# Kernel tuning notes

Hardware: AMD Instinct MI355X
Metric: run time of the kernel (lower is better)

## Reference

```python
import jax, jax.numpy as jnp
import numpy as np

B, S, D = 1, 2048, 2048      # batch, seq, hidden_dim
DF = 768                      # moe intermediate (per routed expert)
DSH = 2048                    # shared-expert intermediate
E, K = 32, 8                  # num routed experts, top_k
BLK = 128                     # fp8 block-scale size
CAP = 1024
T = B * S


def _dequant(w, s, blk=BLK):
    # w: [E, M, N] fp8 values (stored fp32), s: [E, M/blk, N/blk] block scales
    Eh, M, N = w.shape
    Mb, Nb = s.shape[1], s.shape[2]
    return (w.reshape(Eh, Mb, blk, Nb, blk) * s[:, :, None, :, None]).reshape(Eh, M, N)


def setup_inputs() -> dict:
    key = jax.random.key(0)
    ks = jax.random.split(key, 13)
    n = lambda k, shp, sc=0.02: jax.random.normal(k, shp, jnp.float32) * sc
    u = lambda k, shp: jax.random.uniform(k, shp, jnp.float32, 0.005, 0.02)
    return {
        "hidden_states": jax.random.normal(ks[0], (B, S, D), jnp.float32),
        "router_w": n(ks[1], (E, D)),
        # raw fp8-value weights (simulated as fp32 integers-in-range values) + block scale_inv
        "wg_fp8": jax.random.normal(ks[2], (E, DF, D), jnp.float32),
        "sg": u(ks[3], (E, DF // BLK, D // BLK)),
        "wu_fp8": jax.random.normal(ks[4], (E, DF, D), jnp.float32),
        "su": u(ks[5], (E, DF // BLK, D // BLK)),
        "wd_fp8": jax.random.normal(ks[6], (E, D, DF), jnp.float32),
        "sd": u(ks[7], (E, D // BLK, DF // BLK)),
        "ws_gate": n(ks[8], (DSH, D)),
        "ws_up": n(ks[9], (DSH, D)),
        "ws_down": n(ks[10], (D, DSH)),
        "w_shared_gate": n(ks[11], (1, D)),
    }


def reference(hidden_states, router_w, wg_fp8, sg, wu_fp8, su, wd_fp8, sd,
              ws_gate, ws_up, ws_down, w_shared_gate):
    x = hidden_states.reshape(-1, D)  # [T, D]

    # shared expert (SwiGLU) + its sigmoid gate
    shared = (jax.nn.silu(x @ ws_gate.T) * (x @ ws_up.T)) @ ws_down.T
    sh_gate = jax.nn.sigmoid(x @ w_shared_gate.T)  # [T, 1]

    # router: softmax -> top-k -> renormalize (Qwen MoE gate)
    probs = jax.nn.softmax(x @ router_w.T, axis=-1)          # [T, E]
    rw, sel = jax.lax.top_k(probs, K)                        # [T, K]
    rw = rw / jnp.sum(rw, axis=-1, keepdims=True)

    # capacity-based dispatch (replaces the python per-expert loop; same math)
    flat_e = sel.reshape(-1)                                 # [T*K]
    oh = jax.nn.one_hot(flat_e, E, dtype=jnp.int32)
    pos = jnp.sum(jnp.cumsum(oh, axis=0) * oh, axis=-1) - 1  # position within expert
    keep = (pos < CAP)
    pos_c = jnp.minimum(pos, CAP)                            # overflow -> scratch slot CAP
    tok = jnp.arange(T * K) // K                             # owning token of each (t,k) pair

    buf = jnp.zeros((E, CAP + 1, D), x.dtype).at[flat_e, pos_c].set(x[tok])

    # block-scale dequant (fp8*scale_inv), then per-expert SwiGLU
    Wg = _dequant(wg_fp8, sg)
    Wu = _dequant(wu_fp8, su)
    Wd = _dequant(wd_fp8, sd)
    g = jnp.einsum('ecd,efd->ecf', buf, Wg)
    up = jnp.einsum('ecd,efd->ecf', buf, Wu)
    h = jax.nn.silu(g) * up
    y = jnp.einsum('ecf,edf->ecd', h, Wd)                    # [E, CAP+1, D]

    # weighted scatter-add back to tokens (index_add_ equivalent)
    y_tok = y[flat_e, pos_c]                                 # [T*K, D]
    w_tok = rw.reshape(-1) * keep.astype(x.dtype)
    out = jax.ops.segment_sum(y_tok * w_tok[:, None], tok, num_segments=T)

    out = out + sh_gate * shared
    return out.reshape(B, S, D)
```

## Files before the change

### kernel.cpp

```cpp
#include <hip/hip_runtime.h>
#include <hip/hip_bf16.h>


#define TT   2048
#define DD   2048
#define DFF  768
#define DSH  2048
#define EE   32
#define KTOP 8
#define CAP  1024

typedef _Float16 half8  __attribute__((ext_vector_type(8)));
typedef _Float16 half4v __attribute__((ext_vector_type(4)));
typedef float    f32x4  __attribute__((ext_vector_type(4)));

__global__ __launch_bounds__(256) void k_init(int* __restrict__ cnt,
                                              int* __restrict__ slot_tok) {
  int i = blockIdx.x * 256 + threadIdx.x;
  if (i < EE * CAP) slot_tok[i] = 0;
  if (i < EE) cnt[i] = 0;
}

__global__ __launch_bounds__(256) void k_cast(const float* __restrict__ in,
                                              _Float16* __restrict__ out) {
  int i = blockIdx.x * 256 + threadIdx.x;
  float4 v = ((const float4*)in)[i];
  half4v h = { (_Float16)v.x, (_Float16)v.y, (_Float16)v.z, (_Float16)v.w };
  ((half4v*)out)[i] = h;
}

__global__ __launch_bounds__(64) void k_router(
    const float* __restrict__ x, const float* __restrict__ rw,
    const float* __restrict__ wshg,
    float* __restrict__ shg, int* __restrict__ cnt,
    int* __restrict__ slot_tok, float* __restrict__ slot_w,
    int* __restrict__ slot_pair, int* __restrict__ pair_pos) {
  int t = blockIdx.x;
  int lane = threadIdx.x;
  const float* xr = x + (size_t)t * DD;
  float xv[32];
#pragma unroll
  for (int j = 0; j < 32; ++j) xv[j] = xr[lane + j * 64];

  __shared__ float lg[EE];
  for (int e = 0; e < EE; ++e) {
    const float* we = rw + (size_t)e * DD;
    float s = 0.f;
#pragma unroll
    for (int j = 0; j < 32; ++j) s += xv[j] * we[lane + j * 64];
#pragma unroll
    for (int off = 32; off > 0; off >>= 1) s += __shfl_down(s, off);
    if (lane == 0) lg[e] = s;
  }
  {
    float s = 0.f;
#pragma unroll
    for (int j = 0; j < 32; ++j) s += xv[j] * wshg[lane + j * 64];
#pragma unroll
    for (int off = 32; off > 0; off >>= 1) s += __shfl_down(s, off);
    if (lane == 0) shg[t] = 1.f / (1.f + expf(-s));
  }
  if (lane == 0) {
    unsigned used = 0;
    int sel[KTOP];
    float val[KTOP];
    for (int k = 0; k < KTOP; ++k) {
      float bv = -1e30f; int bi = 0;
      for (int e = 0; e < EE; ++e)
        if (!((used >> e) & 1) && lg[e] > bv) { bv = lg[e]; bi = e; }
      used |= (1u << bi);
      sel[k] = bi; val[k] = bv;
    }
    float mx = val[0], sum = 0.f;
    for (int k = 0; k < KTOP; ++k) { val[k] = expf(val[k] - mx); sum += val[k]; }
    float inv = 1.f / sum;
    for (int k = 0; k < KTOP; ++k) {
      int e = sel[k];
      int pos = atomicAdd(&cnt[e], 1);
      pair_pos[t * KTOP + k] = pos;
      if (pos < CAP) {
        slot_tok[e * CAP + pos] = t;
        slot_w[e * CAP + pos] = val[k] * inv;
        slot_pair[e * CAP + pos] = t * KTOP + k;
      }
    }
  }
}

template<bool DUAL, bool GATHER, int EPI, int NPB, int MBB, int KDIM>
__global__ __launch_bounds__(256, 2) void k_gemm(
    const _Float16* __restrict__ A,
    const float* __restrict__ B0f, const float* __restrict__ B1f,
    const float* __restrict__ S0, const float* __restrict__ S1,
    int sCols, int sStrideE,
    _Float16* __restrict__ OutH,
    int ldA, int ldOut,
    long long strideAE, long long strideBE, long long strideOE,
    const int* __restrict__ cnt,
    const int* __restrict__ slot_tok, const float* __restrict__ slot_w) {
  constexpr int BK = 64;
  constexpr int KT = KDIM / BK;
  constexpr int NF = DUAL ? 2 : 4;
  constexpr int BN = DUAL ? 64 : 128;
  constexpr int BCH = DUAL ? 4 : 8;

  const int f = blockIdx.x;
  const int xcd = f & 7;
  const int t0 = f >> 3;
  const int mb = t0 % MBB;
  const int pp = t0 / MBB;
  const int p  = pp * 8 + xcd;
  const int nb = p % NPB;
  const int e  = p / NPB;

  int rows = cnt[e] > CAP ? CAP : cnt[e];
  const int rowBase = mb * 128;
  if (rowBase >= rows) return;
  const int nBase = nb * BN;

  const int tid = threadIdx.x;
  const int lane = tid & 63;
  const int wave = tid >> 6;
  const int wr = wave >> 1;
  const int wc = wave & 1;

  __shared__ __align__(16) _Float16 sA[3][8192];
  __shared__ __align__(16) _Float16 sB[2][8192];

  const _Float16* Ae = A + (GATHER ? 0 : (long long)e * strideAE);
  const float* B0e = B0f + (long long)e * strideBE;
  const float* B1e = DUAL ? (B1f + (long long)e * strideBE) : nullptr;
  const float* S0e = S0 + (long long)e * sStrideE;
  const float* S1e = DUAL ? (S1 + (long long)e * sStrideE) : nullptr;
  const int sRow = (nBase >> 7) * sCols;

  int aByte[4];
#pragma unroll
  for (int i = 0; i < 4; ++i) {
    int c = tid + i * 256;
    int row = c >> 3;
    int colB = ((c & 7) << 4) ^ ((row & 7) << 4);
    int src = GATHER ? slot_tok[e * CAP + rowBase + row] : (rowBase + row);
    aByte[i] = src * (2 * ldA) + colB;
  }
  int bOff[BCH], wByte[BCH];
#pragma unroll
  for (int i = 0; i < BCH; ++i) {
    int c = tid + i * 256;
    int rn = c >> 4;
    int c4 = (c & 15) << 2;
    bOff[i] = (nBase + rn) * KDIM + c4;
    wByte[i] = ((rn << 7) + (c4 << 1)) ^ ((rn & 7) << 4);
  }

  f32x4 accG[4][NF];
  f32x4 accU[DUAL ? 4 : 1][NF];
#pragma unroll
  for (int m = 0; m < 4; ++m)
#pragma unroll
    for (int n = 0; n < NF; ++n) {
      accG[m][n] = (f32x4){0.f, 0.f, 0.f, 0.f};
      if constexpr (DUAL) accU[m][n] = (f32x4){0.f, 0.f, 0.f, 0.f};
    }

  auto stageA = [&](int kt, int buf) {
#pragma unroll
    for (int i = 0; i < 4; ++i) {
      __builtin_amdgcn_global_load_lds(
          (const __attribute__((address_space(1))) void*)
              ((const char*)Ae + aByte[i] + kt * (BK * 2)),
          (__attribute__((address_space(3))) void*)&sA[buf][(tid + i * 256) * 8],
          16, 0, 0);
    }
  };
  auto loadB = [&](int kt, float4 (&r0)[BCH], float4 (&r1)[BCH]) {
    const int ko = kt * BK;
#pragma unroll
    for (int i = 0; i < BCH; ++i) r0[i] = *(const float4*)(B0e + bOff[i] + ko);
    if constexpr (DUAL) {
#pragma unroll
      for (int i = 0; i < BCH; ++i) r1[i] = *(const float4*)(B1e + bOff[i] + ko);
    }
  };
  auto storeB = [&](int kt, float4 (&r0)[BCH], float4 (&r1)[BCH]) {
    float s0 = S0e[sRow + (kt >> 1)];
    float s1 = DUAL ? S1e[sRow + (kt >> 1)] : 0.f;
    char* base = (char*)&sB[kt & 1][0];
#pragma unroll
    for (int i = 0; i < BCH; ++i) {
      half4v h = { (_Float16)(r0[i].x * s0), (_Float16)(r0[i].y * s0),
                   (_Float16)(r0[i].z * s0), (_Float16)(r0[i].w * s0) };
      *(half4v*)(base + wByte[i]) = h;
      if constexpr (DUAL) {
        half4v h1 = { (_Float16)(r1[i].x * s1), (_Float16)(r1[i].y * s1),
                      (_Float16)(r1[i].z * s1), (_Float16)(r1[i].w * s1) };
        *(half4v*)(base + 8192 + wByte[i]) = h1;
      }
    }
  };
  auto computeTile = [&](int ia, int ib) {
    const char* pA = (const char*)&sA[ia][0];
    const char* pB = (const char*)&sB[ib][0];
#pragma unroll
    for (int kk = 0; kk < 2; ++kk) {
      const int koff = kk * 32 + (lane >> 4) * 8;
      half8 a[4];
#pragma unroll
      for (int m = 0; m < 4; ++m) {
        int r = wr * 64 + m * 16 + (lane & 15);
        int byt = ((r << 7) + (koff << 1)) ^ ((r & 7) << 4);
        a[m] = *(const half8*)(pA + byt);
      }
      if constexpr (DUAL) {
        half8 bg[2], bu[2];
#pragma unroll
        for (int n = 0; n < 2; ++n) {
          int rn = wc * 32 + n * 16 + (lane & 15);
          int byt = ((rn << 7) + (koff << 1)) ^ ((rn & 7) << 4);
          bg[n] = *(const half8*)(pB + byt);
          bu[n] = *(const half8*)(pB + 8192 + byt);
        }
#pragma unroll
        for (int m = 0; m < 4; ++m)
#pragma unroll
          for (int n = 0; n < 2; ++n) {
            accG[m][n] = __builtin_amdgcn_mfma_f32_16x16x32_f16(a[m], bg[n], accG[m][n], 0, 0, 0);
            accU[m][n] = __builtin_amdgcn_mfma_f32_16x16x32_f16(a[m], bu[n], accU[m][n], 0, 0, 0);
          }
      } else {
        half8 b[4];
#pragma unroll
        for (int n = 0; n < 4; ++n) {
          int rn = wc * 64 + n * 16 + (lane & 15);
          int byt = ((rn << 7) + (koff << 1)) ^ ((rn & 7) << 4);
          b[n] = *(const half8*)(pB + byt);
        }
#pragma unroll
        for (int m = 0; m < 4; ++m)
#pragma unroll
          for (int n = 0; n < 4; ++n)
            accG[m][n] = __builtin_amdgcn_mfma_f32_16x16x32_f16(a[m], b[n], accG[m][n], 0, 0, 0);
      }
    }
  };

  float4 rbE0[BCH], rbE1[BCH], rbO0[BCH], rbO1[BCH];

  loadB(0, rbE0, rbE1);
  loadB(1, rbO0, rbO1);
  stageA(0, 0);
  stageA(1, 1);
  __builtin_amdgcn_sched_barrier(0);
  storeB(0, rbE0, rbE1);
  asm volatile("s_waitcnt lgkmcnt(0)" ::: "memory");
  asm volatile("s_waitcnt vmcnt(4)" ::: "memory");
  __builtin_amdgcn_s_barrier();
  __builtin_amdgcn_sched_barrier(0);

  int bufC = 0, bufW = 2;
  for (int kt = 0; kt < KT; ++kt) {
    if (kt + 2 < KT) {
      stageA(kt + 2, bufW);
      if (kt & 1) loadB(kt + 2, rbO0, rbO1);
      else        loadB(kt + 2, rbE0, rbE1);
      __builtin_amdgcn_sched_barrier(0);
    }
    computeTile(bufC, kt & 1);
    if (kt + 1 < KT) {
      if (kt & 1) storeB(kt + 1, rbE0, rbE1);
      else        storeB(kt + 1, rbO0, rbO1);
    }
    asm volatile("s_waitcnt lgkmcnt(0)" ::: "memory");
    if (kt + 2 < KT) { asm volatile("s_waitcnt vmcnt(12)" ::: "memory"); }
    else             { asm volatile("s_waitcnt vmcnt(0)"  ::: "memory"); }
    __builtin_amdgcn_s_barrier();
    __builtin_amdgcn_sched_barrier(0);
    bufC = (bufC == 2) ? 0 : bufC + 1;
    bufW = (bufW == 2) ? 0 : bufW + 1;
  }

#pragma unroll
  for (int m = 0; m < 4; ++m) {
#pragma unroll
    for (int i = 0; i < 4; ++i) {
      int row = rowBase + wr * 64 + m * 16 + (lane >> 4) * 4 + i;
      if (row < rows) {
        if constexpr (EPI == 1) {
          int pair = slot_tok[e * CAP + row];
          float w = slot_w[e * CAP + row];
#pragma unroll
          for (int n = 0; n < NF; ++n) {
            int col = nBase + wc * 64 + n * 16 + (lane & 15);
            OutH[(long long)pair * DD + col] = (_Float16)(w * accG[m][n][i]);
          }
        } else {
          long long outBase = (long long)e * strideOE;
#pragma unroll
          for (int n = 0; n < NF; ++n) {
            int col = nBase + (DUAL ? wc * 32 : wc * 64) + n * 16 + (lane & 15);
            long long o = outBase + (long long)row * ldOut + col;
            if constexpr (DUAL) {
              float gv = accG[m][n][i];
              float uv = accU[m][n][i];
              OutH[o] = (_Float16)((gv / (1.f + __expf(-gv))) * uv);
            } else {
              OutH[o] = (_Float16)accG[m][n][i];
            }
          }
        }
      }
    }
  }
}

template<bool DUAL, int EPI, int NPB, int MBB, int KDIM>
__global__ __launch_bounds__(256, 2) void k_gemm16(
    const _Float16* __restrict__ A,
    const _Float16* __restrict__ B0h, const _Float16* __restrict__ B1h,
    _Float16* __restrict__ OutH, float* __restrict__ OutF,
    const float* __restrict__ shg,
    int ldA, int ldOut, int rowsConst) {
  constexpr int BK = 64;
  constexpr int KT = KDIM / BK;
  constexpr int NF = DUAL ? 2 : 4;
  constexpr int BN = DUAL ? 64 : 128;

  const int f = blockIdx.x;
  const int xcd = f & 7;
  const int t0 = f >> 3;
  const int mb = t0 % MBB;
  const int pp = t0 / MBB;
  const int p  = pp * 8 + xcd;
  const int nb = p % NPB;

  int rows = rowsConst;
  const int rowBase = mb * 128;
  if (rowBase >= rows) return;
  const int nBase = nb * BN;

  const int tid = threadIdx.x;
  const int lane = tid & 63;
  const int wave = tid >> 6;
  const int wr = wave >> 1;
  const int wc = wave & 1;

  __shared__ __align__(16) _Float16 sA[3][8192];
  __shared__ __align__(16) _Float16 sB[2][8192];

  int aByte[4];
#pragma unroll
  for (int i = 0; i < 4; ++i) {
    int c = tid + i * 256;
    int row = c >> 3;
    int colB = ((c & 7) << 4) ^ ((row & 7) << 4);
    aByte[i] = (rowBase + row) * (2 * ldA) + colB;
  }
  int bByte[4];
#pragma unroll
  for (int i = 0; i < 4; ++i) {
    int c = tid + i * 256;
    int rn = DUAL ? ((c & 511) >> 3) : (c >> 3);
    int colB = ((c & 7) << 4) ^ ((rn & 7) << 4);
    bByte[i] = (nBase + rn) * (2 * KDIM) + colB;
  }

  f32x4 accG[4][NF];
  f32x4 accU[DUAL ? 4 : 1][NF];
#pragma unroll
  for (int m = 0; m < 4; ++m)
#pragma unroll
    for (int n = 0; n < NF; ++n) {
      accG[m][n] = (f32x4){0.f, 0.f, 0.f, 0.f};
      if constexpr (DUAL) accU[m][n] = (f32x4){0.f, 0.f, 0.f, 0.f};
    }

  auto stageA = [&](int kt, int buf) {
#pragma unroll
    for (int i = 0; i < 4; ++i) {
      __builtin_amdgcn_global_load_lds(
          (const __attribute__((address_space(1))) void*)
              ((const char*)A + aByte[i] + kt * 128),
          (__attribute__((address_space(3))) void*)&sA[buf][(tid + i * 256) * 8],
          16, 0, 0);
    }
  };
  auto stageB = [&](int kt, int buf) {
#pragma unroll
    for (int i = 0; i < 4; ++i) {
      const _Float16* src = (DUAL && i >= 2) ? B1h : B0h;
      __builtin_amdgcn_global_load_lds(
          (const __attribute__((address_space(1))) void*)
              ((const char*)src + bByte[i] + kt * 128),
          (__attribute__((address_space(3))) void*)&sB[buf][(tid + i * 256) * 8],
          16, 0, 0);
    }
  };
  auto computeTile = [&](int ia, int ib) {
    const char* pA = (const char*)&sA[ia][0];
    const char* pB = (const char*)&sB[ib][0];
#pragma unroll
    for (int kk = 0; kk < 2; ++kk) {
      const int koff = kk * 32 + (lane >> 4) * 8;
      half8 a[4];
#pragma unroll
      for (int m = 0; m < 4; ++m) {
        int r = wr * 64 + m * 16 + (lane & 15);
        int byt = ((r << 7) + (koff << 1)) ^ ((r & 7) << 4);
        a[m] = *(const half8*)(pA + byt);
      }
      if constexpr (DUAL) {
        half8 bg[2], bu[2];
#pragma unroll
        for (int n = 0; n < 2; ++n) {
          int rn = wc * 32 + n * 16 + (lane & 15);
          int byt = ((rn << 7) + (koff << 1)) ^ ((rn & 7) << 4);
          bg[n] = *(const half8*)(pB + byt);
          bu[n] = *(const half8*)(pB + 8192 + byt);
        }
#pragma unroll
        for (int m = 0; m < 4; ++m)
#pragma unroll
          for (int n = 0; n < 2; ++n) {
            accG[m][n] = __builtin_amdgcn_mfma_f32_16x16x32_f16(a[m], bg[n], accG[m][n], 0, 0, 0);
            accU[m][n] = __builtin_amdgcn_mfma_f32_16x16x32_f16(a[m], bu[n], accU[m][n], 0, 0, 0);
          }
      } else {
        half8 b[4];
#pragma unroll
        for (int n = 0; n < 4; ++n) {
          int rn = wc * 64 + n * 16 + (lane & 15);
          int byt = ((rn << 7) + (koff << 1)) ^ ((rn & 7) << 4);
          b[n] = *(const half8*)(pB + byt);
        }
#pragma unroll
        for (int m = 0; m < 4; ++m)
#pragma unroll
          for (int n = 0; n < 4; ++n)
            accG[m][n] = __builtin_amdgcn_mfma_f32_16x16x32_f16(a[m], b[n], accG[m][n], 0, 0, 0);
      }
    }
  };

  stageB(0, 0);
  __builtin_amdgcn_sched_barrier(0);
  stageA(0, 0);
  __builtin_amdgcn_sched_barrier(0);
  stageA(1, 1);
  __builtin_amdgcn_sched_barrier(0);

  int bufC = 0, bufW = 2;
  for (int kt = 0; kt < KT; ++kt) {
    asm volatile("s_waitcnt lgkmcnt(0)" ::: "memory");
    if (kt + 1 < KT) { asm volatile("s_waitcnt vmcnt(4)" ::: "memory"); }
    else             { asm volatile("s_waitcnt vmcnt(0)" ::: "memory"); }
    __builtin_amdgcn_sched_barrier(0);
    __builtin_amdgcn_s_barrier();
    __builtin_amdgcn_sched_barrier(0);
    if (kt + 1 < KT) stageB(kt + 1, (kt + 1) & 1);
    if (kt + 2 < KT) stageA(kt + 2, bufW);
    __builtin_amdgcn_sched_barrier(0);
    computeTile(bufC, kt & 1);
    bufC = (bufC == 2) ? 0 : bufC + 1;
    bufW = (bufW == 2) ? 0 : bufW + 1;
  }

#pragma unroll
  for (int m = 0; m < 4; ++m) {
#pragma unroll
    for (int i = 0; i < 4; ++i) {
      int row = rowBase + wr * 64 + m * 16 + (lane >> 4) * 4 + i;
      if (row < rows) {
        if constexpr (EPI == 2) {
          float g = shg[row];
#pragma unroll
          for (int n = 0; n < NF; ++n) {
            int col = nBase + wc * 64 + n * 16 + (lane & 15);
            OutF[(long long)row * DD + col] += g * accG[m][n][i];
          }
        } else {
#pragma unroll
          for (int n = 0; n < NF; ++n) {
            int col = nBase + (DUAL ? wc * 32 : wc * 64) + n * 16 + (lane & 15);
            long long o = (long long)row * ldOut + col;
            if constexpr (DUAL) {
              float gv = accG[m][n][i];
              float uv = accU[m][n][i];
              OutH[o] = (_Float16)((gv / (1.f + __expf(-gv))) * uv);
            } else {
              OutH[o] = (_Float16)accG[m][n][i];
            }
          }
        }
      }
    }
  }
}

__global__ __launch_bounds__(256) void k_combine(
    const _Float16* __restrict__ Yp, const int* __restrict__ pair_pos,
    float* __restrict__ out) {
  int t = blockIdx.x;
  int col = threadIdx.x * 8;
  float acc[8] = {0.f, 0.f, 0.f, 0.f, 0.f, 0.f, 0.f, 0.f};
#pragma unroll
  for (int k = 0; k < KTOP; ++k) {
    if (pair_pos[t * KTOP + k] < CAP) {
      half8 y = *(const half8*)&Yp[((size_t)t * KTOP + k) * DD + col];
#pragma unroll
      for (int j = 0; j < 8; ++j) acc[j] += (float)y[j];
    }
  }
  float4 o0 = {acc[0], acc[1], acc[2], acc[3]};
  float4 o1 = {acc[4], acc[5], acc[6], acc[7]};
  *(float4*)&out[(size_t)t * DD + col] = o0;
  *(float4*)&out[(size_t)t * DD + col + 4] = o1;
}

extern "C" void kernel_launch(void* const* d_in, const int* in_sizes, int n_in,
                              void* d_out, int out_size, void* d_ws, size_t ws_size,
                              hipStream_t stream) {
  (void)in_sizes; (void)n_in; (void)out_size; (void)ws_size;
  const float* x    = (const float*)d_in[0];
  const float* rw   = (const float*)d_in[1];
  const float* wg   = (const float*)d_in[2];
  const float* sg   = (const float*)d_in[3];
  const float* wu   = (const float*)d_in[4];
  const float* su   = (const float*)d_in[5];
  const float* wd   = (const float*)d_in[6];
  const float* sd   = (const float*)d_in[7];
  const float* wsg  = (const float*)d_in[8];
  const float* wsu  = (const float*)d_in[9];
  const float* wsd  = (const float*)d_in[10];
  const float* wshg = (const float*)d_in[11];
  float* out = (float*)d_out;

  char* p = (char*)d_ws;
  auto alloc = [&](size_t bytes) {
    char* r = p;
    p += (bytes + 255) & ~(size_t)255;
    return r;
  };
  _Float16* x_h   = (_Float16*)alloc((size_t)TT * DD * 2);
  _Float16* H     = (_Float16*)alloc((size_t)EE * CAP * DFF * 2);
  _Float16* Hsh   = (_Float16*)alloc((size_t)TT * DSH * 2);
  _Float16* Yp    = (_Float16*)alloc((size_t)TT * KTOP * DD * 2);
  _Float16* wsg_h = (_Float16*)alloc((size_t)DSH * DD * 2);
  _Float16* wsu_h = (_Float16*)alloc((size_t)DSH * DD * 2);
  _Float16* wsd_h = (_Float16*)alloc((size_t)DD * DSH * 2);
  float* shg      = (float*)alloc((size_t)TT * 4);
  int* cnt        = (int*)alloc((size_t)EE * 4);
  int* slot_tok   = (int*)alloc((size_t)EE * CAP * 4);
  float* slot_w   = (float*)alloc((size_t)EE * CAP * 4);
  int* slot_pair  = (int*)alloc((size_t)EE * CAP * 4);
  int* pair_pos   = (int*)alloc((size_t)TT * KTOP * 4);

  k_init<<<(EE * CAP + 255) / 256, 256, 0, stream>>>(cnt, slot_tok);
  k_cast<<<(TT * DD / 4) / 256, 256, 0, stream>>>(x, x_h);
  k_cast<<<(DSH * DD / 4) / 256, 256, 0, stream>>>(wsg, wsg_h);
  k_cast<<<(DSH * DD / 4) / 256, 256, 0, stream>>>(wsu, wsu_h);
  k_cast<<<(DD * DSH / 4) / 256, 256, 0, stream>>>(wsd, wsd_h);
  k_router<<<TT, 64, 0, stream>>>(x, rw, wshg, shg, cnt, slot_tok, slot_w,
                                  slot_pair, pair_pos);

  k_gemm<true, true, 0, 12, 8, DD><<<3072, 256, 0, stream>>>(
      x_h, wg, wu, sg, su, DD / 128, (DFF / 128) * (DD / 128),
      H, DD, DFF,
      0LL, (long long)DFF * DD, (long long)CAP * DFF,
      cnt, slot_tok, nullptr);

  k_gemm<false, false, 1, 16, 8, DFF><<<4096, 256, 0, stream>>>(
      H, wd, wd, sd, sd, DFF / 128, (DD / 128) * (DFF / 128),
      Yp, DFF, DD,
      (long long)CAP * DFF, (long long)DD * DFF, 0LL,
      cnt, slot_pair, slot_w);

  k_combine<<<TT, 256, 0, stream>>>(Yp, pair_pos, out);

  k_gemm16<true, 0, 32, 16, DD><<<512, 256, 0, stream>>>(
      x_h, wsg_h, wsu_h, Hsh, nullptr, nullptr,
      DD, DSH, TT);

  k_gemm16<false, 2, 16, 16, DSH><<<256, 256, 0, stream>>>(
      Hsh, wsd_h, wsd_h, nullptr, out, shg,
      DSH, DD, TT);
}
```

Measured before the change: 762.2 us.

## Fold weight dequant/cast into idle gate-up GEMM blocks via work pool

Early-exit and finished blocks of the gate/up expert GEMM now pull chunks from an atomic work counter and use them to dequantize the down-projection weights and cast the shared-expert weights to fp16. This lets the separate cast kernels go away. The down-projection GEMM then runs on the pre-dequantized fp16 weights through the generic fp16 GEMM path, which was extended to handle per-expert strides and gather. The gate/up pipeline is also restructured into a two-step unrolled loop with different wait and barrier placement. The cost is a larger fp16 workspace, extra writes of the dequantized weights, and added work at the tail of the GEMM kernel.

```diff
diff --git a/kernel.cpp b/kernel.cpp
--- a/kernel.cpp
+++ b/kernel.cpp
@@ -14,11 +14,18 @@
 typedef _Float16 half4v __attribute__((ext_vector_type(4)));
 typedef float    f32x4  __attribute__((ext_vector_type(4)));
 
+#define N4_WD  12582912LL
+#define N4_SH  1048576LL
+#define PCHUNK 8192
+#define NCHUNK 1920
+
 __global__ __launch_bounds__(256) void k_init(int* __restrict__ cnt,
-                                              int* __restrict__ slot_tok) {
+                                              int* __restrict__ slot_tok,
+                                              int* __restrict__ ctr) {
   int i = blockIdx.x * 256 + threadIdx.x;
   if (i < EE * CAP) slot_tok[i] = 0;
   if (i < EE) cnt[i] = 0;
+  if (i == 0) *ctr = 0;
 }
 
 __global__ __launch_bounds__(256) void k_cast(const float* __restrict__ in,
@@ -87,22 +94,69 @@
   }
 }
 
-template<bool DUAL, bool GATHER, int EPI, int NPB, int MBB, int KDIM>
-__global__ __launch_bounds__(256, 2) void k_gemm(
+__device__ __forceinline__ void pool_fn(
+    int tid, int* lds_c, int* ctr,
+    const float* __restrict__ wd, const float* __restrict__ sd,
+    _Float16* __restrict__ wd_h,
+    const float* __restrict__ wsg, const float* __restrict__ wsu,
+    const float* __restrict__ wsd,
+    _Float16* __restrict__ wsg_h, _Float16* __restrict__ wsu_h,
+    _Float16* __restrict__ wsd_h) {
+  __syncthreads();
+  for (;;) {
+    if (tid == 0) *lds_c = atomicAdd(ctr, 1);
+    __syncthreads();
+    int c = *lds_c;
+    __syncthreads();
+    if (c >= NCHUNK) return;
+    long long base = (long long)c * PCHUNK;
+    for (int j = 0; j < PCHUNK / 256; ++j) {
+      long long idx = base + tid + j * 256;
+      if (idx < N4_WD) {
+        long long b = idx * 4;
+        int e = (int)(b / ((long long)DD * DFF));
+        int rem = (int)(b - (long long)e * DD * DFF);
+        int r = rem / DFF;
+        int col = rem - r * DFF;
+        float sc = sd[e * ((DD / 128) * (DFF / 128)) +
+                      (r >> 7) * (DFF / 128) + (col >> 7)];
+        float4 v = ((const float4*)wd)[idx];
+        half4v h = { (_Float16)(v.x * sc), (_Float16)(v.y * sc),
+                     (_Float16)(v.z * sc), (_Float16)(v.w * sc) };
+        ((half4v*)wd_h)[idx] = h;
+      } else {
+        long long i2 = idx - N4_WD;
+        const float* src; _Float16* dst;
+        if (i2 < N4_SH)            { src = wsg; dst = wsg_h; }
+        else if (i2 < 2 * N4_SH)   { src = wsu; dst = wsu_h; i2 -= N4_SH; }
+        else                       { src = wsd; dst = wsd_h; i2 -= 2 * N4_SH; }
+        float4 v = ((const float4*)src)[i2];
+        half4v h = { (_Float16)v.x, (_Float16)v.y, (_Float16)v.z, (_Float16)v.w };
+        ((half4v*)dst)[i2] = h;
+      }
+    }
+  }
+}
+
+template<int NPB, int MBB, int KDIM>
+__global__ __launch_bounds__(256, 2) void k_gemm_gu(
     const _Float16* __restrict__ A,
     const float* __restrict__ B0f, const float* __restrict__ B1f,
     const float* __restrict__ S0, const float* __restrict__ S1,
     int sCols, int sStrideE,
     _Float16* __restrict__ OutH,
-    int ldA, int ldOut,
-    long long strideAE, long long strideBE, long long strideOE,
-    const int* __restrict__ cnt,
-    const int* __restrict__ slot_tok, const float* __restrict__ slot_w) {
+    int ldA, int ldOut, long long strideBE, long long strideOE,
+    const int* __restrict__ cnt, const int* __restrict__ slot_tok,
+    int* __restrict__ ctr,
+    const float* __restrict__ pwd, const float* __restrict__ psd,
+    _Float16* __restrict__ pwd_h,
+    const float* __restrict__ pwsg, const float* __restrict__ pwsu,
+    const float* __restrict__ pwsd,
+    _Float16* __restrict__ pwsg_h, _Float16* __restrict__ pwsu_h,
+    _Float16* __restrict__ pwsd_h) {
   constexpr int BK = 64;
   constexpr int KT = KDIM / BK;
-  constexpr int NF = DUAL ? 2 : 4;
-  constexpr int BN = DUAL ? 64 : 128;
-  constexpr int BCH = DUAL ? 4 : 8;
+  constexpr int BCH = 4;
 
   const int f = blockIdx.x;
   const int xcd = f & 7;
@@ -113,25 +167,30 @@
   const int nb = p % NPB;
   const int e  = p / NPB;
 
+  const int tid = threadIdx.x;
+
+  __shared__ __align__(16) _Float16 sA[3][8192];
+  __shared__ __align__(16) _Float16 sB[2][8192];
+  int* lds_c = (int*)&sA[0][0];
+
   int rows = cnt[e] > CAP ? CAP : cnt[e];
   const int rowBase = mb * 128;
-  if (rowBase >= rows) return;
-  const int nBase = nb * BN;
-
-  const int tid = threadIdx.x;
+  if (rowBase >= rows) {
+    pool_fn(tid, lds_c, ctr, pwd, psd, pwd_h, pwsg, pwsu, pwsd,
+            pwsg_h, pwsu_h, pwsd_h);
+    return;
+  }
+  const int nBase = nb * 64;
+
   const int lane = tid & 63;
   const int wave = tid >> 6;
   const int wr = wave >> 1;
   const int wc = wave & 1;
 
-  __shared__ __align__(16) _Float16 sA[3][8192];
-  __shared__ __align__(16) _Float16 sB[2][8192];
-
-  const _Float16* Ae = A + (GATHER ? 0 : (long long)e * strideAE);
   const float* B0e = B0f + (long long)e * strideBE;
-  const float* B1e = DUAL ? (B1f + (long long)e * strideBE) : nullptr;
+  const float* B1e = B1f + (long long)e * strideBE;
   const float* S0e = S0 + (long long)e * sStrideE;
-  const float* S1e = DUAL ? (S1 + (long long)e * sStrideE) : nullptr;
+  const float* S1e = S1 + (long long)e * sStrideE;
   const int sRow = (nBase >> 7) * sCols;
 
   int aByte[4];
@@ -140,7 +199,7 @@
     int c = tid + i * 256;
     int row = c >> 3;
     int colB = ((c & 7) << 4) ^ ((row & 7) << 4);
-    int src = GATHER ? slot_tok[e * CAP + rowBase + row] : (rowBase + row);
+    int src = slot_tok[e * CAP + rowBase + row];
     aByte[i] = src * (2 * ldA) + colB;
   }
   int bOff[BCH], wByte[BCH];
@@ -153,14 +212,13 @@
     wByte[i] = ((rn << 7) + (c4 << 1)) ^ ((rn & 7) << 4);
   }
 
-  f32x4 accG[4][NF];
-  f32x4 accU[DUAL ? 4 : 1][NF];
+  f32x4 accG[4][2], accU[4][2];
 #pragma unroll
   for (int m = 0; m < 4; ++m)
 #pragma unroll
-    for (int n = 0; n < NF; ++n) {
+    for (int n = 0; n < 2; ++n) {
       accG[m][n] = (f32x4){0.f, 0.f, 0.f, 0.f};
-      if constexpr (DUAL) accU[m][n] = (f32x4){0.f, 0.f, 0.f, 0.f};
+      accU[m][n] = (f32x4){0.f, 0.f, 0.f, 0.f};
     }
 
   auto stageA = [&](int kt, int buf) {
@@ -168,7 +226,7 @@
     for (int i = 0; i < 4; ++i) {
       __builtin_amdgcn_global_load_lds(
           (const __attribute__((address_space(1))) void*)
-              ((const char*)Ae + aByte[i] + kt * (BK * 2)),
+              ((const char*)A + aByte[i] + kt * (BK * 2)),
           (__attribute__((address_space(3))) void*)&sA[buf][(tid + i * 256) * 8],
           16, 0, 0);
     }
@@ -177,25 +235,21 @@
     const int ko = kt * BK;
 #pragma unroll
     for (int i = 0; i < BCH; ++i) r0[i] = *(const float4*)(B0e + bOff[i] + ko);
-    if constexpr (DUAL) {
-#pragma unroll
-      for (int i = 0; i < BCH; ++i) r1[i] = *(const float4*)(B1e + bOff[i] + ko);
-    }
+#pragma unroll
+    for (int i = 0; i < BCH; ++i) r1[i] = *(const float4*)(B1e + bOff[i] + ko);
   };
   auto storeB = [&](int kt, float4 (&r0)[BCH], float4 (&r1)[BCH]) {
     float s0 = S0e[sRow + (kt >> 1)];
-    float s1 = DUAL ? S1e[sRow + (kt >> 1)] : 0.f;
+    float s1 = S1e[sRow + (kt >> 1)];
     char* base = (char*)&sB[kt & 1][0];
 #pragma unroll
     for (int i = 0; i < BCH; ++i) {
       half4v h = { (_Float16)(r0[i].x * s0), (_Float16)(r0[i].y * s0),
                    (_Float16)(r0[i].z * s0), (_Float16)(r0[i].w * s0) };
       *(half4v*)(base + wByte[i]) = h;
-      if constexpr (DUAL) {
-        half4v h1 = { (_Float16)(r1[i].x * s1), (_Float16)(r1[i].y * s1),
-                      (_Float16)(r1[i].z * s1), (_Float16)(r1[i].w * s1) };
-        *(half4v*)(base + 8192 + wByte[i]) = h1;
-      }
+      half4v h1 = { (_Float16)(r1[i].x * s1), (_Float16)(r1[i].y * s1),
+                    (_Float16)(r1[i].z * s1), (_Float16)(r1[i].w * s1) };
+      *(half4v*)(base + 8192 + wByte[i]) = h1;
     }
   };
   auto computeTile = [&](int ia, int ib) {
@@ -211,70 +265,58 @@
         int byt = ((r << 7) + (koff << 1)) ^ ((r & 7) << 4);
         a[m] = *(const half8*)(pA + byt);
       }
-      if constexpr (DUAL) {
-        half8 bg[2], bu[2];
+      half8 bg[2], bu[2];
+#pragma unroll
+      for (int n = 0; n < 2; ++n) {
+        int rn = wc * 32 + n * 16 + (lane & 15);
+        int byt = ((rn << 7) + (koff << 1)) ^ ((rn & 7) << 4);
+        bg[n] = *(const half8*)(pB + byt);
+        bu[n] = *(const half8*)(pB + 8192 + byt);
+      }
+#pragma unroll
+      for (int m = 0; m < 4; ++m)
 #pragma unroll
         for (int n = 0; n < 2; ++n) {
-          int rn = wc * 32 + n * 16 + (lane & 15);
-          int byt = ((rn << 7) + (koff << 1)) ^ ((rn & 7) << 4);
-          bg[n] = *(const half8*)(pB + byt);
-          bu[n] = *(const half8*)(pB + 8192 + byt);
+          accG[m][n] = __builtin_amdgcn_mfma_f32_16x16x32_f16(a[m], bg[n], accG[m][n], 0, 0, 0);
+          accU[m][n] = __builtin_amdgcn_mfma_f32_16x16x32_f16(a[m], bu[n], accU[m][n], 0, 0, 0);
         }
-#pragma unroll
-        for (int m = 0; m < 4; ++m)
-#pragma unroll
-          for (int n = 0; n < 2; ++n) {
-            accG[m][n] = __builtin_amdgcn_mfma_f32_16x16x32_f16(a[m], bg[n], accG[m][n], 0, 0, 0);
-            accU[m][n] = __builtin_amdgcn_mfma_f32_16x16x32_f16(a[m], bu[n], accU[m][n], 0, 0, 0);
-          }
-      } else {
-        half8 b[4];
-#pragma unroll
-        for (int n = 0; n < 4; ++n) {
-          int rn = wc * 64 + n * 16 + (lane & 15);
-          int byt = ((rn << 7) + (koff << 1)) ^ ((rn & 7) << 4);
-          b[n] = *(const half8*)(pB + byt);
-        }
-#pragma unroll
-        for (int m = 0; m < 4; ++m)
-#pragma unroll
-          for (int n = 0; n < 4; ++n)
-            accG[m][n] = __builtin_amdgcn_mfma_f32_16x16x32_f16(a[m], b[n], accG[m][n], 0, 0, 0);
-      }
     }
   };
 
   float4 rbE0[BCH], rbE1[BCH], rbO0[BCH], rbO1[BCH];
 
-  loadB(0, rbE0, rbE1);
-  loadB(1, rbO0, rbO1);
-  stageA(0, 0);
-  stageA(1, 1);
+  stageA(0, 0); loadB(0, rbE0, rbE1);
   __builtin_amdgcn_sched_barrier(0);
-  storeB(0, rbE0, rbE1);
-  asm volatile("s_waitcnt lgkmcnt(0)" ::: "memory");
-  asm volatile("s_waitcnt vmcnt(4)" ::: "memory");
-  __builtin_amdgcn_s_barrier();
+  stageA(1, 1); loadB(1, rbO0, rbO1);
   __builtin_amdgcn_sched_barrier(0);
 
   int bufC = 0, bufW = 2;
-  for (int kt = 0; kt < KT; ++kt) {
-    if (kt + 2 < KT) {
-      stageA(kt + 2, bufW);
-      if (kt & 1) loadB(kt + 2, rbO0, rbO1);
-      else        loadB(kt + 2, rbE0, rbE1);
-      __builtin_amdgcn_sched_barrier(0);
-    }
-    computeTile(bufC, kt & 1);
-    if (kt + 1 < KT) {
-      if (kt & 1) storeB(kt + 1, rbE0, rbE1);
-      else        storeB(kt + 1, rbO0, rbO1);
-    }
+  for (int kt = 0; kt < KT; kt += 2) {
+    if (kt + 1 < KT) { asm volatile("s_waitcnt vmcnt(12)" ::: "memory"); }
+    else             { asm volatile("s_waitcnt vmcnt(0)"  ::: "memory"); }
+    __builtin_amdgcn_sched_barrier(0);
+    storeB(kt, rbE0, rbE1);
     asm volatile("s_waitcnt lgkmcnt(0)" ::: "memory");
+    __builtin_amdgcn_sched_barrier(0);
+    __builtin_amdgcn_s_barrier();
+    __builtin_amdgcn_sched_barrier(0);
+    if (kt + 2 < KT) { stageA(kt + 2, bufW); loadB(kt + 2, rbE0, rbE1); }
+    __builtin_amdgcn_sched_barrier(0);
+    computeTile(bufC, 0);
+    bufC = (bufC == 2) ? 0 : bufC + 1;
+    bufW = (bufW == 2) ? 0 : bufW + 1;
+
     if (kt + 2 < KT) { asm volatile("s_waitcnt vmcnt(12)" ::: "memory"); }
     else             { asm volatile("s_waitcnt vmcnt(0)"  ::: "memory"); }
+    __builtin_amdgcn_sched_barrier(0);
+    storeB(kt + 1, rbO0, rbO1);
+    asm volatile("s_waitcnt lgkmcnt(0)" ::: "memory");
+    __builtin_amdgcn_sched_barrier(0);
     __builtin_amdgcn_s_barrier();
     __builtin_amdgcn_sched_barrier(0);
+    if (kt + 3 < KT) { stageA(kt + 3, bufW); loadB(kt + 3, rbO0, rbO1); }
+    __builtin_amdgcn_sched_barrier(0);
+    computeTile(bufC, 1);
     bufC = (bufC == 2) ? 0 : bufC + 1;
     bufW = (bufW == 2) ? 0 : bufW + 1;
   }
@@ -285,43 +327,33 @@
     for (int i = 0; i < 4; ++i) {
       int row = rowBase + wr * 64 + m * 16 + (lane >> 4) * 4 + i;
       if (row < rows) {
-        if constexpr (EPI == 1) {
-          int pair = slot_tok[e * CAP + row];
-          float w = slot_w[e * CAP + row];
-#pragma unroll
-          for (int n = 0; n < NF; ++n) {
-            int col = nBase + wc * 64 + n * 16 + (lane & 15);
-            OutH[(long long)pair * DD + col] = (_Float16)(w * accG[m][n][i]);
-          }
-        } else {
-          long long outBase = (long long)e * strideOE;
-#pragma unroll
-          for (int n = 0; n < NF; ++n) {
-            int col = nBase + (DUAL ? wc * 32 : wc * 64) + n * 16 + (lane & 15);
-            long long o = outBase + (long long)row * ldOut + col;
-            if constexpr (DUAL) {
-              float gv = accG[m][n][i];
-              float uv = accU[m][n][i];
-              OutH[o] = (_Float16)((gv / (1.f + __expf(-gv))) * uv);
-            } else {
-              OutH[o] = (_Float16)accG[m][n][i];
-            }
-          }
+#pragma unroll
+        for (int n = 0; n < 2; ++n) {
+          int col = nBase + wc * 32 + n * 16 + (lane & 15);
+          float gv = accG[m][n][i];
+          float uv = accU[m][n][i];
+          OutH[(long long)e * strideOE + (long long)row * ldOut + col] =
+              (_Float16)((gv / (1.f + __expf(-gv))) * uv);
         }
       }
     }
   }
-}
-
-template<bool DUAL, int EPI, int NPB, int MBB, int KDIM>
+
+  pool_fn(tid, lds_c, ctr, pwd, psd, pwd_h, pwsg, pwsu, pwsd,
+          pwsg_h, pwsu_h, pwsd_h);
+}
+
+template<bool DUAL, bool GATHER, int EPI, int NPB, int MBB, int KDIM>
 __global__ __launch_bounds__(256, 2) void k_gemm16(
     const _Float16* __restrict__ A,
     const _Float16* __restrict__ B0h, const _Float16* __restrict__ B1h,
     _Float16* __restrict__ OutH, float* __restrict__ OutF,
     const float* __restrict__ shg,
-    int ldA, int ldOut, int rowsConst) {
-  constexpr int BK = 64;
-  constexpr int KT = KDIM / BK;
+    int ldA, int ldOut,
+    long long strideAE, long long strideBE, long long strideOE,
+    const int* __restrict__ cnt, int rowsConst,
+    const int* __restrict__ slot_tok, const float* __restrict__ slot_w) {
+  constexpr int KT = KDIM / 64;
   constexpr int NF = DUAL ? 2 : 4;
   constexpr int BN = DUAL ? 64 : 128;
 
@@ -332,8 +364,9 @@
   const int pp = t0 / MBB;
   const int p  = pp * 8 + xcd;
   const int nb = p % NPB;
-
-  int rows = rowsConst;
+  const int e  = p / NPB;
+
+  int rows = cnt ? (cnt[e] > CAP ? CAP : cnt[e]) : rowsConst;
   const int rowBase = mb * 128;
   if (rowBase >= rows) return;
   const int nBase = nb * BN;
@@ -347,13 +380,18 @@
   __shared__ __align__(16) _Float16 sA[3][8192];
   __shared__ __align__(16) _Float16 sB[2][8192];
 
+  const _Float16* Ae = A + (GATHER ? 0 : (long long)e * strideAE);
+  const _Float16* B0e = B0h + (long long)e * strideBE;
+  const _Float16* B1e = DUAL ? (B1h + (long long)e * strideBE) : nullptr;
+
   int aByte[4];
 #pragma unroll
   for (int i = 0; i < 4; ++i) {
     int c = tid + i * 256;
     int row = c >> 3;
     int colB = ((c & 7) << 4) ^ ((row & 7) << 4);
-    aByte[i] = (rowBase + row) * (2 * ldA) + colB;
+    int src = GATHER ? slot_tok[e * CAP + rowBase + row] : (rowBase + row);
+    aByte[i] = src * (2 * ldA) + colB;
   }
   int bByte[4];
 #pragma unroll
@@ -379,7 +417,7 @@
     for (int i = 0; i < 4; ++i) {
       __builtin_amdgcn_global_load_lds(
           (const __attribute__((address_space(1))) void*)
-              ((const char*)A + aByte[i] + kt * 128),
+              ((const char*)Ae + aByte[i] + kt * 128),
           (__attribute__((address_space(3))) void*)&sA[buf][(tid + i * 256) * 8],
           16, 0, 0);
     }
@@ -387,7 +425,7 @@
   auto stageB = [&](int kt, int buf) {
 #pragma unroll
     for (int i = 0; i < 4; ++i) {
-      const _Float16* src = (DUAL && i >= 2) ? B1h : B0h;
+      const _Float16* src = (DUAL && i >= 2) ? B1e : B0e;
       __builtin_amdgcn_global_load_lds(
           (const __attribute__((address_space(1))) void*)
               ((const char*)src + bByte[i] + kt * 128),
@@ -470,7 +508,15 @@
     for (int i = 0; i < 4; ++i) {
       int row = rowBase + wr * 64 + m * 16 + (lane >> 4) * 4 + i;
       if (row < rows) {
-        if constexpr (EPI == 2) {
+        if constexpr (EPI == 1) {
+          int pair = slot_tok[e * CAP + row];
+          float w = slot_w[e * CAP + row];
+#pragma unroll
+          for (int n = 0; n < NF; ++n) {
+            int col = nBase + wc * 64 + n * 16 + (lane & 15);
+            OutH[(long long)pair * DD + col] = (_Float16)(w * accG[m][n][i]);
+          }
+        } else if constexpr (EPI == 2) {
           float g = shg[row];
 #pragma unroll
           for (int n = 0; n < NF; ++n) {
@@ -478,10 +524,11 @@
             OutF[(long long)row * DD + col] += g * accG[m][n][i];
           }
         } else {
+          long long outBase = (long long)e * strideOE;
 #pragma unroll
           for (int n = 0; n < NF; ++n) {
             int col = nBase + (DUAL ? wc * 32 : wc * 64) + n * 16 + (lane & 15);
-            long long o = (long long)row * ldOut + col;
+            long long o = outBase + (long long)row * ldOut + col;
             if constexpr (DUAL) {
               float gv = accG[m][n][i];
               float uv = accU[m][n][i];
@@ -544,6 +591,7 @@
   _Float16* H     = (_Float16*)alloc((size_t)EE * CAP * DFF * 2);
   _Float16* Hsh   = (_Float16*)alloc((size_t)TT * DSH * 2);
   _Float16* Yp    = (_Float16*)alloc((size_t)TT * KTOP * DD * 2);
+  _Float16* wd_h  = (_Float16*)alloc((size_t)EE * DD * DFF * 2);
   _Float16* wsg_h = (_Float16*)alloc((size_t)DSH * DD * 2);
   _Float16* wsu_h = (_Float16*)alloc((size_t)DSH * DD * 2);
   _Float16* wsd_h = (_Float16*)alloc((size_t)DD * DSH * 2);
@@ -553,34 +601,34 @@
   float* slot_w   = (float*)alloc((size_t)EE * CAP * 4);
   int* slot_pair  = (int*)alloc((size_t)EE * CAP * 4);
   int* pair_pos   = (int*)alloc((size_t)TT * KTOP * 4);
-
-  k_init<<<(EE * CAP + 255) / 256, 256, 0, stream>>>(cnt, slot_tok);
+  int* ctr        = (int*)alloc(256);
+
+  k_init<<<(EE * CAP + 255) / 256, 256, 0, stream>>>(cnt, slot_tok, ctr);
   k_cast<<<(TT * DD / 4) / 256, 256, 0, stream>>>(x, x_h);
-  k_cast<<<(DSH * DD / 4) / 256, 256, 0, stream>>>(wsg, wsg_h);
-  k_cast<<<(DSH * DD / 4) / 256, 256, 0, stream>>>(wsu, wsu_h);
-  k_cast<<<(DD * DSH / 4) / 256, 256, 0, stream>>>(wsd, wsd_h);
   k_router<<<TT, 64, 0, stream>>>(x, rw, wshg, shg, cnt, slot_tok, slot_w,
                                   slot_pair, pair_pos);
 
-  k_gemm<true, true, 0, 12, 8, DD><<<3072, 256, 0, stream>>>(
+  k_gemm_gu<12, 8, DD><<<3072, 256, 0, stream>>>(
       x_h, wg, wu, sg, su, DD / 128, (DFF / 128) * (DD / 128),
-      H, DD, DFF,
-      0LL, (long long)DFF * DD, (long long)CAP * DFF,
-      cnt, slot_tok, nullptr);
-
-  k_gemm<false, false, 1, 16, 8, DFF><<<4096, 256, 0, stream>>>(
-      H, wd, wd, sd, sd, DFF / 128, (DD / 128) * (DFF / 128),
-      Yp, DFF, DD,
+      H, DD, DFF, (long long)DFF * DD, (long long)CAP * DFF,
+      cnt, slot_tok,
+      ctr, wd, sd, wd_h, wsg, wsu, wsd, wsg_h, wsu_h, wsd_h);
+
+  k_gemm16<false, false, 1, 16, 8, DFF><<<4096, 256, 0, stream>>>(
+      H, wd_h, wd_h, Yp, nullptr, nullptr,
+      DFF, DD,
       (long long)CAP * DFF, (long long)DD * DFF, 0LL,
-      cnt, slot_pair, slot_w);
+      cnt, 0, slot_pair, slot_w);
 
   k_combine<<<TT, 256, 0, stream>>>(Yp, pair_pos, out);
 
-  k_gemm16<true, 0, 32, 16, DD><<<512, 256, 0, stream>>>(
+  k_gemm16<true, false, 0, 32, 16, DD><<<512, 256, 0, stream>>>(
       x_h, wsg_h, wsu_h, Hsh, nullptr, nullptr,
-      DD, DSH, TT);
-
-  k_gemm16<false, 2, 16, 16, DSH><<<256, 256, 0, stream>>>(
+      DD, DSH, 0LL, 0LL, 0LL,
+      nullptr, TT, nullptr, nullptr);
+
+  k_gemm16<false, false, 2, 16, 16, DSH><<<256, 256, 0, stream>>>(
       Hsh, wsd_h, wsd_h, nullptr, out, shg,
-      DSH, DD, TT);
-}
+      DSH, DD, 0LL, 0LL, 0LL,
+      nullptr, TT, nullptr, nullptr);
+}
```

Result: faster. 712.6 us (-6.5%).
